# Kernel optimization log

Measured on AMD Instinct MI355X. Metric: run time of the kernel, lower is better.

## Reference

```python
import math
import jax, jax.numpy as jnp
import numpy as np


def _pairwise_sqdist(x, y):
    # x: [N, d], y: [M, d] -> [N, M]
    x2 = jnp.sum(x * x, axis=-1)[:, None]
    y2 = jnp.sum(y * y, axis=-1)[None, :]
    return jnp.maximum(x2 + y2 - 2.0 * (x @ y.T), 0.0)


def setup_inputs() -> dict:
    key = jax.random.key(0)
    k1, k2 = jax.random.split(key)
    N, M, D = 8192, 8192, 2
    base_points = jax.random.normal(k1, (N, D), dtype=jnp.float32)
    target_points = jax.random.normal(k2, (M, D), dtype=jnp.float32)
    log_sigma = jnp.asarray(math.log(0.1), dtype=jnp.float32)
    log_scale = jnp.zeros((D,), dtype=jnp.float32)
    return {
        "base_points": base_points,
        "target_points": target_points,
        "log_sigma": log_sigma,
        "log_scale": log_scale,
    }


def reference(base_points, target_points, log_sigma, log_scale):
    # learn_scale=True: anisotropic per-coordinate scaling
    scale = jnp.exp(log_scale)
    base = base_points * scale
    target = target_points * scale

    # uniform node weights (use_weight_net=False)
    N = base.shape[0]
    M = target.shape[0]
    w_base = jnp.full((N,), 1.0 / N, dtype=base.dtype)
    w_target = jnp.full((M,), 1.0 / M, dtype=target.dtype)

    # center=True: subtract weighted centroid of each cloud
    base = base - jnp.sum(w_base[:, None] * base, axis=0, keepdims=True)
    target = target - jnp.sum(w_target[:, None] * target, axis=0, keepdims=True)

    sigma = jnp.exp(log_sigma)
    inv2s2 = 1.0 / (2.0 * sigma * sigma)

    k_bb = jnp.exp(-_pairwise_sqdist(base, base) * inv2s2)      # [N, N]
    k_tt = jnp.exp(-_pairwise_sqdist(target, target) * inv2s2)  # [M, M]
    k_bt = jnp.exp(-_pairwise_sqdist(base, target) * inv2s2)    # [N, M]

    term_bb = w_base @ (k_bb @ w_base)
    term_tt = w_target @ (k_tt @ w_target)
    term_bt = w_base @ (k_bt @ w_target)
    loss = term_bb + term_tt - 2.0 * term_bt
    return loss
```

## Files before the change

### kernel.cpp

```cpp
#include <hip/hip_runtime.h>


#define BLOCK 256
#define NT_CROSS 2048
#define NT_TOT   4160
#define LOG2E 1.4426950408889634f

typedef float v2f __attribute__((ext_vector_type(2)));

struct Prep { float f0, f1, sh0, sh1; };

__device__ __forceinline__ float fexp2(float x) {
    return __builtin_amdgcn_exp2f(x);
}

__global__ __launch_bounds__(1024) void prep_kernel(
    const float* __restrict__ base, const float* __restrict__ target,
    const float* __restrict__ log_sigma, const float* __restrict__ log_scale,
    int N, int M, Prep* __restrict__ pp, double* __restrict__ slots)
{
    __shared__ double mred[16][4];
    const int tid = threadIdx.x;
    if (tid < 64) slots[tid] = 0.0;

    double sbx = 0, sby = 0, stx = 0, sty = 0;
    const float4* b4 = (const float4*)base;
    const float4* t4 = (const float4*)target;
    for (int i = tid; i < (N >> 1); i += 1024) {
        float4 v = b4[i];
        sbx += (double)v.x + (double)v.z;
        sby += (double)v.y + (double)v.w;
    }
    for (int i = tid; i < (M >> 1); i += 1024) {
        float4 v = t4[i];
        stx += (double)v.x + (double)v.z;
        sty += (double)v.y + (double)v.w;
    }
    for (int off = 32; off; off >>= 1) {
        sbx += __shfl_down(sbx, off); sby += __shfl_down(sby, off);
        stx += __shfl_down(stx, off); sty += __shfl_down(sty, off);
    }
    if ((tid & 63) == 0) {
        mred[tid >> 6][0] = sbx; mred[tid >> 6][1] = sby;
        mred[tid >> 6][2] = stx; mred[tid >> 6][3] = sty;
    }
    __syncthreads();
    if (tid == 0) {
        double b0 = 0, b1 = 0, t0 = 0, t1 = 0;
        for (int k = 0; k < 16; ++k) {
            b0 += mred[k][0]; b1 += mred[k][1];
            t0 += mred[k][2]; t1 += mred[k][3];
        }
        float s0 = expf(log_scale[0]);
        float s1 = expf(log_scale[1]);
        float sigma = expf(log_sigma[0]);
        float inv2s2 = 1.0f / (2.0f * sigma * sigma);
        float sq = sqrtf(inv2s2 * LOG2E);
        float f0 = s0 * sq, f1 = s1 * sq;
        pp->f0 = f0; pp->f1 = f1;
        pp->sh0 = (float)(b0 / (double)N - t0 / (double)M) * f0;
        pp->sh1 = (float)(b1 / (double)N - t1 / (double)M) * f1;
    }
}

__global__ __launch_bounds__(BLOCK, 8) void mmd_main(
    const float* __restrict__ base, const float* __restrict__ target,
    int N, int M, const Prep* __restrict__ pp, double* __restrict__ slots)
{
    __shared__ __align__(16) float tbx[256];
    __shared__ __align__(16) float tby[256];
    __shared__ __align__(16) float tbc[256];
    __shared__ double wredd[4];

    const int tid = threadIdx.x;
    const int t   = blockIdx.x;
    const Prep p = *pp;
    const float2* base2   = (const float2*)base;
    const float2* target2 = (const float2*)target;

    const double wNN = 1.0 / ((double)N * (double)N);
    const double wMM = 1.0 / ((double)M * (double)M);
    const double wNM = -2.0 / ((double)N * (double)M);

    int ib, jb;
    bool diag;
    int term;
    const float2* A2;
    const float2* B2;
    double wt;
    float shx = 0.f, shy = 0.f;
    if (t < NT_CROSS) {
        ib = t >> 5; jb = t & 31;
        A2 = base2; B2 = target2;
        wt = wNM; diag = false; term = 2;
        shx = p.sh0; shy = p.sh1;
    } else {
        const int u = t - NT_CROSS;
        term = (u >= 1056) ? 1 : 0;
        const int v = u - term * 1056;
        int q = (int)((65.0f - sqrtf(4225.0f - 4.0f * (float)v)) * 0.5f);
        q = min(max(q, 0), 31);
        while (q > 0 && (65 * q - q * q) > v) --q;
        while (q < 31 && (65 * (q + 1) - (q + 1) * (q + 1)) <= v) ++q;
        const int r = v - (65 * q - q * q);
        const int cnt = 32 - q;
        ib = 2 * q + (r >= cnt ? 1 : 0);
        jb = q + (r >= cnt ? r - cnt : r);
        diag = (jb == q);
        A2 = term ? target2 : base2;  B2 = A2;
        wt = 2.0 * (term ? wMM : wNN);
    }
    const int i0 = ib * 128, j0 = jb * 256;

    {
        float2 b = B2[j0 + tid];
        float bx = b.x * p.f0, by = b.y * p.f1;
        tbx[tid] = bx;
        tby[tid] = by;
        tbc[tid] = -fmaf(bx, bx, by * by);
    }
    __syncthreads();

    const int row = i0 + (tid & 127);
    const int js  = (tid >> 7) * 128;
    float2 a = A2[row];
    const float ax = fmaf(a.x, p.f0, -shx);
    const float ay = fmaf(a.y, p.f1, -shy);
    const float ax2 = ax + ax, ay2 = ay + ay;
    const float A0 = -fmaf(ax, ax, ay * ay);

    const float4* bx4 = (const float4*)(tbx + js);
    const float4* by4 = (const float4*)(tby + js);
    const float4* c4  = (const float4*)(tbc + js);

    double result;
    if (!diag) {
        const v2f ax2v = { ax2, ax2 };
        const v2f ay2v = { ay2, ay2 };
        const v2f A0v  = { A0, A0 };
        v2f s01 = { 0.f, 0.f }, s23 = { 0.f, 0.f };
#pragma unroll 4
        for (int q = 0; q < 32; ++q) {
            float4 BX = bx4[q];
            float4 BY = by4[q];
            float4 C  = c4[q];
            v2f bx01 = { BX.x, BX.y }, bx23 = { BX.z, BX.w };
            v2f by01 = { BY.x, BY.y }, by23 = { BY.z, BY.w };
            v2f c01  = { C.x,  C.y  }, c23  = { C.z,  C.w  };
            v2f e01 = ax2v * bx01 + (ay2v * by01 + (c01 + A0v));
            v2f e23 = ax2v * bx23 + (ay2v * by23 + (c23 + A0v));
            v2f x01 = { fexp2(e01.x), fexp2(e01.y) };
            v2f x23 = { fexp2(e23.x), fexp2(e23.y) };
            s01 += x01;
            s23 += x23;
        }
        v2f st = s01 + s23;
        result = wt * (double)(st.x + st.y);
    } else {
        float sge = 0.f, sgt = 0.f;
        const int jbase = j0 + js;
#pragma unroll 2
        for (int q = 0; q < 32; ++q) {
            float4 BX = bx4[q];
            float4 BY = by4[q];
            float4 C  = c4[q];
            float e0 = fmaf(ax2, BX.x, fmaf(ay2, BY.x, C.x + A0));
            float e1 = fmaf(ax2, BX.y, fmaf(ay2, BY.y, C.y + A0));
            float e2 = fmaf(ax2, BX.z, fmaf(ay2, BY.z, C.z + A0));
            float e3 = fmaf(ax2, BX.w, fmaf(ay2, BY.w, C.w + A0));
            float v0 = fexp2(e0), v1 = fexp2(e1);
            float v2 = fexp2(e2), v3 = fexp2(e3);
            const int j = jbase + 4 * q;
            sge += (j + 0 >= row) ? v0 : 0.f;  sgt += (j + 0 > row) ? v0 : 0.f;
            sge += (j + 1 >= row) ? v1 : 0.f;  sgt += (j + 1 > row) ? v1 : 0.f;
            sge += (j + 2 >= row) ? v2 : 0.f;  sgt += (j + 2 > row) ? v2 : 0.f;
            sge += (j + 3 >= row) ? v3 : 0.f;  sgt += (j + 3 > row) ? v3 : 0.f;
        }
        result = (term ? wMM : wNN) * (double)(sge + sgt);
    }

    for (int off = 32; off; off >>= 1) result += __shfl_down(result, off);
    if ((tid & 63) == 0) wredd[tid >> 6] = result;
    __syncthreads();
    if (tid == 0) {
        double s = wredd[0] + wredd[1] + wredd[2] + wredd[3];
        atomicAdd(&slots[t & 63], s);
    }
}

__global__ void final_kernel(const double* __restrict__ slots,
                             float* __restrict__ out)
{
    const int tid = threadIdx.x;
    double s = slots[tid];
    for (int off = 32; off; off >>= 1) s += __shfl_down(s, off);
    if (tid == 0) out[0] = (float)s;
}

extern "C" void kernel_launch(void* const* d_in, const int* in_sizes, int n_in,
                              void* d_out, int out_size, void* d_ws, size_t ws_size,
                              hipStream_t stream)
{
    const float* base      = (const float*)d_in[0];
    const float* target    = (const float*)d_in[1];
    const float* log_sigma = (const float*)d_in[2];
    const float* log_scale = (const float*)d_in[3];
    float* out = (float*)d_out;

    int N = in_sizes[0] / 2;
    int M = in_sizes[1] / 2;

    Prep*   pp    = (Prep*)d_ws;
    double* slots = (double*)((char*)d_ws + 64);

    prep_kernel<<<1, 1024, 0, stream>>>(base, target, log_sigma, log_scale,
                                        N, M, pp, slots);
    mmd_main<<<NT_TOT, BLOCK, 0, stream>>>(base, target, N, M, pp, slots);
    final_kernel<<<1, 64, 0, stream>>>(slots, out);
}
```

Before: 91.81 us.

## Compute four rows per thread to enlarge tiles and amortize LDS reads

Each block now covers 512 rows instead of 128, with every thread handling four rows against the same shared-memory column tile. The triangular tile enumeration for the self-terms is reworked for the new 512x256 tile shape, and the block count falls to 1056. This amortizes LDS loads and per-block setup across more exp evaluations. In exchange it raises register use (launch bounds drop to 4 waves), cuts the number of blocks, and sends more work through the masked diagonal path.

```diff
diff --git a/kernel.cpp b/kernel.cpp
--- a/kernel.cpp
+++ b/kernel.cpp
@@ -2,8 +2,8 @@
 
 
 #define BLOCK 256
-#define NT_CROSS 2048
-#define NT_TOT   4160
+#define NT_CROSS 512
+#define NT_TOT   1056
 #define LOG2E 1.4426950408889634f
 
 typedef float v2f __attribute__((ext_vector_type(2)));
@@ -63,7 +63,7 @@
     }
 }
 
-__global__ __launch_bounds__(BLOCK, 8) void mmd_main(
+__global__ __launch_bounds__(BLOCK, 4) void mmd_main(
     const float* __restrict__ base, const float* __restrict__ target,
     int N, int M, const Prep* __restrict__ pp, double* __restrict__ slots)
 {
@@ -82,9 +82,8 @@
     const double wMM = 1.0 / ((double)M * (double)M);
     const double wNM = -2.0 / ((double)N * (double)M);
 
-    int ib, jb;
+    int ib, jb, term;
     bool diag;
-    int term;
     const float2* A2;
     const float2* B2;
     double wt;
@@ -96,21 +95,19 @@
         shx = p.sh0; shy = p.sh1;
     } else {
         const int u = t - NT_CROSS;
-        term = (u >= 1056) ? 1 : 0;
-        const int v = u - term * 1056;
-        int q = (int)((65.0f - sqrtf(4225.0f - 4.0f * (float)v)) * 0.5f);
-        q = min(max(q, 0), 31);
-        while (q > 0 && (65 * q - q * q) > v) --q;
-        while (q < 31 && (65 * (q + 1) - (q + 1) * (q + 1)) <= v) ++q;
-        const int r = v - (65 * q - q * q);
-        const int cnt = 32 - q;
-        ib = 2 * q + (r >= cnt ? 1 : 0);
-        jb = q + (r >= cnt ? r - cnt : r);
-        diag = (jb == q);
+        term = (u >= 272) ? 1 : 0;
+        const int v = u - term * 272;
+        int r = (int)((33.0f - sqrtf(1089.0f - 4.0f * (float)v)) * 0.5f);
+        r = min(max(r, 0), 15);
+        while (r > 0 && r * (33 - r) > v) --r;
+        while (r < 15 && (r + 1) * (32 - r) <= v) ++r;
+        ib = r;
+        jb = 2 * r + (v - r * (33 - r));
+        diag = (jb <= 2 * r + 1);
         A2 = term ? target2 : base2;  B2 = A2;
         wt = 2.0 * (term ? wMM : wNN);
     }
-    const int i0 = ib * 128, j0 = jb * 256;
+    const int i0 = ib * 512, j0 = jb * 256;
 
     {
         float2 b = B2[j0 + tid];
@@ -121,13 +118,19 @@
     }
     __syncthreads();
 
-    const int row = i0 + (tid & 127);
+    const int r0  = i0 + (tid & 127);
     const int js  = (tid >> 7) * 128;
-    float2 a = A2[row];
-    const float ax = fmaf(a.x, p.f0, -shx);
-    const float ay = fmaf(a.y, p.f1, -shy);
-    const float ax2 = ax + ax, ay2 = ay + ay;
-    const float A0 = -fmaf(ax, ax, ay * ay);
+
+    float ax2s[4], ay2s[4], A0s[4];
+#pragma unroll
+    for (int k = 0; k < 4; ++k) {
+        float2 a = A2[r0 + 128 * k];
+        float ax = fmaf(a.x, p.f0, -shx);
+        float ay = fmaf(a.y, p.f1, -shy);
+        ax2s[k] = ax + ax;
+        ay2s[k] = ay + ay;
+        A0s[k]  = -fmaf(ax, ax, ay * ay);
+    }
 
     const float4* bx4 = (const float4*)(tbx + js);
     const float4* by4 = (const float4*)(tby + js);
@@ -135,10 +138,9 @@
 
     double result;
     if (!diag) {
-        const v2f ax2v = { ax2, ax2 };
-        const v2f ay2v = { ay2, ay2 };
-        const v2f A0v  = { A0, A0 };
-        v2f s01 = { 0.f, 0.f }, s23 = { 0.f, 0.f };
+        v2f s[4][2];
+#pragma unroll
+        for (int k = 0; k < 4; ++k) { s[k][0] = (v2f){0.f, 0.f}; s[k][1] = (v2f){0.f, 0.f}; }
 #pragma unroll 4
         for (int q = 0; q < 32; ++q) {
             float4 BX = bx4[q];
@@ -147,15 +149,24 @@
             v2f bx01 = { BX.x, BX.y }, bx23 = { BX.z, BX.w };
             v2f by01 = { BY.x, BY.y }, by23 = { BY.z, BY.w };
             v2f c01  = { C.x,  C.y  }, c23  = { C.z,  C.w  };
-            v2f e01 = ax2v * bx01 + (ay2v * by01 + (c01 + A0v));
-            v2f e23 = ax2v * bx23 + (ay2v * by23 + (c23 + A0v));
-            v2f x01 = { fexp2(e01.x), fexp2(e01.y) };
-            v2f x23 = { fexp2(e23.x), fexp2(e23.y) };
-            s01 += x01;
-            s23 += x23;
-        }
-        v2f st = s01 + s23;
-        result = wt * (double)(st.x + st.y);
+#pragma unroll
+            for (int k = 0; k < 4; ++k) {
+                v2f A0v  = { A0s[k],  A0s[k]  };
+                v2f ax2v = { ax2s[k], ax2s[k] };
+                v2f ay2v = { ay2s[k], ay2s[k] };
+                v2f e01 = ax2v * bx01 + (ay2v * by01 + (c01 + A0v));
+                v2f e23 = ax2v * bx23 + (ay2v * by23 + (c23 + A0v));
+                s[k][0] += (v2f){ fexp2(e01.x), fexp2(e01.y) };
+                s[k][1] += (v2f){ fexp2(e23.x), fexp2(e23.y) };
+            }
+        }
+        double tot = 0.0;
+#pragma unroll
+        for (int k = 0; k < 4; ++k) {
+            v2f st = s[k][0] + s[k][1];
+            tot += (double)(st.x + st.y);
+        }
+        result = wt * tot;
     } else {
         float sge = 0.f, sgt = 0.f;
         const int jbase = j0 + js;
@@ -164,17 +175,21 @@
             float4 BX = bx4[q];
             float4 BY = by4[q];
             float4 C  = c4[q];
-            float e0 = fmaf(ax2, BX.x, fmaf(ay2, BY.x, C.x + A0));
-            float e1 = fmaf(ax2, BX.y, fmaf(ay2, BY.y, C.y + A0));
-            float e2 = fmaf(ax2, BX.z, fmaf(ay2, BY.z, C.z + A0));
-            float e3 = fmaf(ax2, BX.w, fmaf(ay2, BY.w, C.w + A0));
-            float v0 = fexp2(e0), v1 = fexp2(e1);
-            float v2 = fexp2(e2), v3 = fexp2(e3);
             const int j = jbase + 4 * q;
-            sge += (j + 0 >= row) ? v0 : 0.f;  sgt += (j + 0 > row) ? v0 : 0.f;
-            sge += (j + 1 >= row) ? v1 : 0.f;  sgt += (j + 1 > row) ? v1 : 0.f;
-            sge += (j + 2 >= row) ? v2 : 0.f;  sgt += (j + 2 > row) ? v2 : 0.f;
-            sge += (j + 3 >= row) ? v3 : 0.f;  sgt += (j + 3 > row) ? v3 : 0.f;
+#pragma unroll
+            for (int k = 0; k < 4; ++k) {
+                const int row = r0 + 128 * k;
+                float e0 = fmaf(ax2s[k], BX.x, fmaf(ay2s[k], BY.x, C.x + A0s[k]));
+                float e1 = fmaf(ax2s[k], BX.y, fmaf(ay2s[k], BY.y, C.y + A0s[k]));
+                float e2 = fmaf(ax2s[k], BX.z, fmaf(ay2s[k], BY.z, C.z + A0s[k]));
+                float e3 = fmaf(ax2s[k], BX.w, fmaf(ay2s[k], BY.w, C.w + A0s[k]));
+                float v0 = fexp2(e0), v1 = fexp2(e1);
+                float v2 = fexp2(e2), v3 = fexp2(e3);
+                sge += (j + 0 >= row) ? v0 : 0.f;  sgt += (j + 0 > row) ? v0 : 0.f;
+                sge += (j + 1 >= row) ? v1 : 0.f;  sgt += (j + 1 > row) ? v1 : 0.f;
+                sge += (j + 2 >= row) ? v2 : 0.f;  sgt += (j + 2 > row) ? v2 : 0.f;
+                sge += (j + 3 >= row) ? v3 : 0.f;  sgt += (j + 3 > row) ? v3 : 0.f;
+            }
         }
         result = (term ? wMM : wNN) * (double)(sge + sgt);
     }
```

Result: slower. 100.3 us (+9.2%).
